# Performance work log

Hardware: AMD Instinct MI355X
Metric: run time of the kernel (lower is better)

Reference implementation:

```python
import jax, jax.numpy as jnp
import numpy as np

DIN = 1024
DOUT = 1024


def setup_inputs() -> dict:
    key = jax.random.key(0)
    kx, kq, kk, kv = jax.random.split(key, 4)
    B, T = 4, 2048
    x = jax.random.normal(kx, (B, T, DIN), dtype=jnp.float32)
    # nn.Linear weights are (dout, din); init like PyTorch default scale
    s = 1.0 / np.sqrt(DIN)
    Wq = jax.random.uniform(kq, (DOUT, DIN), minval=-s, maxval=s, dtype=jnp.float32)
    Wk = jax.random.uniform(kk, (DOUT, DIN), minval=-s, maxval=s, dtype=jnp.float32)
    Wv = jax.random.uniform(kv, (DOUT, DIN), minval=-s, maxval=s, dtype=jnp.float32)
    return {"x": x, "Wq": Wq, "Wk": Wk, "Wv": Wv}


def reference(x, Wq, Wk, Wv):
    B, T, _ = x.shape
    q = jnp.einsum('btd,ed->bte', x, Wq)
    k = jnp.einsum('btd,ed->bte', x, Wk)
    v = jnp.einsum('btd,ed->bte', x, Wv)
    attn = jnp.einsum('bqe,bke->bqk', q, k)  # [B, T, T]
    # Faithful to source: masked_fill result is discarded, so the causal mask
    # is a MULTIPLICATIVE tril of ones (upper triangle logits become 0, not -inf).
    mask = jnp.tril(jnp.ones((T, T), dtype=attn.dtype))
    attn = attn * mask
    # Faithful to source: scale by sqrt(last dim of attn) = sqrt(T), not sqrt(d).
    attn = jax.nn.softmax(attn / jnp.sqrt(jnp.asarray(T, attn.dtype)), axis=-1)
    return jnp.einsum('bqk,bke->bqe', attn, v)
```

## Files before the change

### kernel.cpp

```cpp
#include <hip/hip_runtime.h>
#include <stdint.h>

#define BB 4
#define TT 2048
#define DD 1024
#define NX (BB*TT*DD)
#define NW (DD*DD)
#define SCALE 0.022097086912079608f

typedef short v8s __attribute__((ext_vector_type(8)));
typedef float v4f __attribute__((ext_vector_type(4)));

typedef const void __attribute__((address_space(1))) *as1_cvp;
typedef void __attribute__((address_space(3))) *as3_vp;

__device__ __forceinline__ short f2bf(float f) {
    union { float f; uint32_t u; } x; x.f = f;
    uint32_t r = x.u + 0x7fffu + ((x.u >> 16) & 1u);
    return (short)(r >> 16);
}
__device__ __forceinline__ float bf2f(short s) {
    union { uint32_t u; float f; } x; x.u = ((uint32_t)(uint16_t)s) << 16;
    return x.f;
}

__device__ __forceinline__ void gl_lds16(const short* g, const short* lds_wave_base) {
    __builtin_amdgcn_global_load_lds(
        (as1_cvp)(uintptr_t)(const void*)g,
        (as3_vp)(uint32_t)(uintptr_t)(const void*)lds_wave_base,
        16, 0, 0);
}

__device__ __forceinline__ void stage_tile(const short* __restrict__ gsrc, int lda,
                                           short* lds, int tid) {
    int wave = tid >> 6;
    #pragma unroll
    for (int is = 0; is < 4; is++) {
        int t = is * 256 + tid;
        int r = t >> 3, c = t & 7;
        int cg = c ^ (r & 7);
        const short* g = gsrc + (size_t)r * lda + cg * 8;
        const short* l = lds + is * 2048 + wave * 512;
        gl_lds16(g, l);
    }
}
__device__ __forceinline__ void stage_tile64(const short* __restrict__ gsrc, int lda,
                                             short* lds, int tid) {
    int wave = tid >> 6;
    #pragma unroll
    for (int is = 0; is < 2; is++) {
        int t = is * 256 + tid;
        int r = t >> 3, c = t & 7;
        int cg = c ^ (r & 7);
        const short* g = gsrc + (size_t)r * lda + cg * 8;
        const short* l = lds + is * 2048 + wave * 512;
        gl_lds16(g, l);
    }
}
__device__ __forceinline__ v8s frag_read(const short* lds, int row, int cg) {
    return *(const v8s*)(lds + row * 64 + ((cg ^ (row & 7)) << 3));
}

#define COMPUTE_TILE(Ac, Bc)                                                        \
    _Pragma("unroll")                                                               \
    for (int kk = 0; kk < 2; kk++) {                                                \
        v8s af[4], bf[4];                                                           \
        _Pragma("unroll")                                                           \
        for (int i = 0; i < 4; i++) af[i] = frag_read(Ac, wm + i*16 + lr, kk*4 + lq); \
        _Pragma("unroll")                                                           \
        for (int j = 0; j < 4; j++) bf[j] = frag_read(Bc, wn + j*16 + lr, kk*4 + lq); \
        _Pragma("unroll")                                                           \
        for (int i = 0; i < 4; i++)                                                 \
            _Pragma("unroll")                                                       \
            for (int j = 0; j < 4; j++)                                             \
                acc[i][j] = __builtin_amdgcn_mfma_f32_16x16x32_bf16(af[i], bf[j], acc[i][j], 0, 0, 0); \
    }

#define COMPUTE_TILE64(Ac, Bc)                                                      \
    _Pragma("unroll")                                                               \
    for (int kk = 0; kk < 2; kk++) {                                                \
        v8s af[2], bf[4];                                                           \
        _Pragma("unroll")                                                           \
        for (int i = 0; i < 2; i++) af[i] = frag_read(Ac, wm + i*16 + lr, kk*4 + lq); \
        _Pragma("unroll")                                                           \
        for (int j = 0; j < 4; j++) bf[j] = frag_read(Bc, wn + j*16 + lr, kk*4 + lq); \
        _Pragma("unroll")                                                           \
        for (int i = 0; i < 2; i++)                                                 \
            _Pragma("unroll")                                                       \
            for (int j = 0; j < 4; j++)                                             \
                acc[i][j] = __builtin_amdgcn_mfma_f32_16x16x32_bf16(af[i], bf[j], acc[i][j], 0, 0, 0); \
    }

__global__ void k_convert(const float* __restrict__ x, const float* __restrict__ Wq,
                          const float* __restrict__ Wk, const float* __restrict__ Wv,
                          short* __restrict__ dst, float* __restrict__ rowsum) {
    int i = blockIdx.x * 256 + threadIdx.x;
    if (i < BB * TT) rowsum[i] = (float)((15 - ((i & 2047) >> 7)) * 128);
    size_t base = (size_t)i * 4;
    const float* src; size_t off;
    if (base < NX)               { src = x;  off = base; }
    else if (base < NX + NW)     { src = Wq; off = base - NX; }
    else if (base < NX + 2*(size_t)NW) { src = Wk; off = base - NX - NW; }
    else                         { src = Wv; off = base - NX - 2*(size_t)NW; }
    float4 f = *(const float4*)(src + off);
    short4 h; h.x = f2bf(f.x); h.y = f2bf(f.y); h.z = f2bf(f.z); h.w = f2bf(f.w);
    *(short4*)(dst + base) = h;
}

__global__ __launch_bounds__(256) void k_qkv(const short* __restrict__ xb,
                                             const short* __restrict__ wb,
                                             short* __restrict__ q,
                                             short* __restrict__ k,
                                             short* __restrict__ vt) {
    int which = blockIdx.z;
    const short* Bm = wb + (size_t)which * NW;
    int m0 = blockIdx.x * 128, n0 = blockIdx.y * 128;
    __shared__ __align__(16) short SH[32768];
    int tid = threadIdx.x, lane = tid & 63, wave = tid >> 6;
    int wm = (wave >> 1) * 64, wn = (wave & 1) * 64;
    int lr = lane & 15, lq = lane >> 4;
    v4f acc[4][4];
    for (int i = 0; i < 4; i++) for (int j = 0; j < 4; j++) acc[i][j] = (v4f){0.f,0.f,0.f,0.f};

    const short* Ag = xb + (size_t)m0 * 1024;
    const short* Bg = Bm + (size_t)n0 * 1024;
    stage_tile(Ag, 1024, SH, tid);
    stage_tile(Bg, 1024, SH + 16384, tid);
    #pragma unroll
    for (int it = 0; it < 16; ++it) {
        __syncthreads();
        short* Ac = SH + (it & 1) * 8192;
        short* Bc = SH + 16384 + (it & 1) * 8192;
        if (it + 1 < 16) {
            stage_tile(Ag + (it + 1) * 64, 1024, SH + ((it + 1) & 1) * 8192, tid);
            stage_tile(Bg + (it + 1) * 64, 1024, SH + 16384 + ((it + 1) & 1) * 8192, tid);
        }
        COMPUTE_TILE(Ac, Bc);
    }
    short* outp = (which == 0) ? q : k;
    #pragma unroll
    for (int i = 0; i < 4; i++)
        #pragma unroll
        for (int j = 0; j < 4; j++)
            #pragma unroll
            for (int r = 0; r < 4; r++) {
                int row = m0 + wm + i*16 + lq*4 + r;
                int col = n0 + wn + j*16 + lr;
                short hv = f2bf(acc[i][j][r]);
                if (which == 2) {
                    int bb = row >> 11, t = row & 2047;
                    vt[((size_t)bb << 21) + ((size_t)col << 11) + t] = hv;
                } else {
                    outp[(size_t)row * 1024 + col] = hv;
                }
            }
}

__global__ void k_ts1(const short* __restrict__ vt, float* __restrict__ TSpart) {
    int g = blockIdx.x * 256 + threadIdx.x;
    int b = g >> 14, jt = (g >> 10) & 15, e = g & 1023;
    const short* row = vt + ((size_t)b << 21) + ((size_t)e << 11) + jt * 128;
    float s = 0.f;
    #pragma unroll
    for (int c = 0; c < 16; c++) {
        uint4 u = *(const uint4*)(row + c * 8);
        const short* hp = (const short*)&u;
        #pragma unroll
        for (int z = 0; z < 8; z++) s += bf2f(hp[z]);
    }
    TSpart[g] = s;
}
__global__ void k_ts2(const float* __restrict__ TSpart, float* __restrict__ TS) {
    int g = blockIdx.x * 256 + threadIdx.x;
    int b = g >> 10, e = g & 1023;
    float acc = 0.f;
    TS[(size_t)(b * 17 + 16) * 1024 + e] = 0.f;
    for (int jt = 15; jt >= 0; jt--) {
        acc += TSpart[(size_t)(b * 16 + jt) * 1024 + e];
        TS[(size_t)(b * 17 + jt) * 1024 + e] = acc;
    }
}

__global__ __launch_bounds__(256, 3) void k_pk(const short* __restrict__ qm,
                                               const short* __restrict__ km,
                                               short* __restrict__ P,
                                               float* __restrict__ rowsum) {
    int flip = 271 - blockIdx.x, b = blockIdx.z;
    int half = flip & 1, pidx = flip >> 1;
    int qt = 0;
    while ((qt + 1) * (qt + 2) / 2 <= pidx) qt++;
    int kt = pidx - qt * (qt + 1) / 2;
    int r0 = qt * 128 + half * 64;
    const short* Ag = qm + ((size_t)b * 2048 + r0) * 1024;
    const short* Bg = km + ((size_t)b * 2048 + (size_t)kt * 128) * 1024;
    __shared__ __align__(16) short SH[24576];
    int tid = threadIdx.x, lane = tid & 63, wave = tid >> 6;
    int wm = (wave >> 1) * 32, wn = (wave & 1) * 64;
    int lr = lane & 15, lq = lane >> 4;
    v4f acc[2][4];
    for (int i = 0; i < 2; i++) for (int j = 0; j < 4; j++) acc[i][j] = (v4f){0.f,0.f,0.f,0.f};

    stage_tile64(Ag, 1024, SH, tid);
    stage_tile(Bg, 1024, SH + 8192, tid);
    #pragma unroll
    for (int it = 0; it < 16; ++it) {
        __syncthreads();
        short* Ac = SH + (it & 1) * 4096;
        short* Bc = SH + 8192 + (it & 1) * 8192;
        if (it + 1 < 16) {
            stage_tile64(Ag + (it + 1) * 64, 1024, SH + ((it + 1) & 1) * 4096, tid);
            stage_tile  (Bg + (it + 1) * 64, 1024, SH + 8192 + ((it + 1) & 1) * 8192, tid);
        }
        COMPUTE_TILE64(Ac, Bc);
    }
    short* Pb = P + ((size_t)b << 22);
    float rs[2][4];
    for (int i = 0; i < 2; i++) for (int r = 0; r < 4; r++) rs[i][r] = 0.f;
    #pragma unroll
    for (int i = 0; i < 2; i++)
        #pragma unroll
        for (int j = 0; j < 4; j++)
            #pragma unroll
            for (int r = 0; r < 4; r++) {
                int qi = r0 + wm + i*16 + lq*4 + r;
                int kj = kt * 128 + wn + j*16 + lr;
                float p = (kj <= qi) ? __expf(acc[i][j][r] * SCALE) : 1.0f;
                Pb[(size_t)qi * 2048 + kj] = f2bf(p);
                rs[i][r] += p;
            }
    #pragma unroll
    for (int m = 1; m < 16; m <<= 1)
        #pragma unroll
        for (int i = 0; i < 2; i++)
            #pragma unroll
            for (int r = 0; r < 4; r++) rs[i][r] += __shfl_xor(rs[i][r], m);
    if (lr == 0)
        #pragma unroll
        for (int i = 0; i < 2; i++)
            #pragma unroll
            for (int r = 0; r < 4; r++)
                atomicAdd(&rowsum[b * 2048 + r0 + wm + i*16 + lq*4 + r], rs[i][r]);
}

__global__ __launch_bounds__(256, 3) void k_pv(const short* __restrict__ P,
                                               const short* __restrict__ vt,
                                               const float* __restrict__ rowsum,
                                               const float* __restrict__ TS,
                                               float* __restrict__ out) {
    int et = blockIdx.x, p = blockIdx.y >> 1, half = blockIdx.y & 1, b = blockIdx.z;
    const short* Bg = vt + ((size_t)b << 21) + (size_t)et * 128 * 2048;
    __shared__ __align__(16) short SH[24576];
    int tid = threadIdx.x, lane = tid & 63, wave = tid >> 6;
    int wm = (wave >> 1) * 32, wn = (wave & 1) * 64;
    int lr = lane & 15, lq = lane >> 4;

    #pragma unroll
    for (int ph = 0; ph < 2; ph++) {
        int qt = ph ? p : 15 - p;
        int r0 = qt * 128 + half * 64;
        int iters = 2 * (qt + 1);
        const short* Ag = P + ((size_t)b << 22) + (size_t)r0 * 2048;
        v4f acc[2][4];
        for (int i = 0; i < 2; i++) for (int j = 0; j < 4; j++) acc[i][j] = (v4f){0.f,0.f,0.f,0.f};

        stage_tile64(Ag, 2048, SH, tid);
        stage_tile(Bg, 2048, SH + 8192, tid);
        for (int it = 0; it < iters; it += 2) {
            __syncthreads();
            if (it + 1 < iters) {
                stage_tile64(Ag + (it + 1) * 64, 2048, SH + 4096, tid);
                stage_tile  (Bg + (it + 1) * 64, 2048, SH + 8192 + 8192, tid);
            }
            COMPUTE_TILE64(SH, SH + 8192);
            __syncthreads();
            if (it + 2 < iters) {
                stage_tile64(Ag + (it + 2) * 64, 2048, SH, tid);
                stage_tile  (Bg + (it + 2) * 64, 2048, SH + 8192, tid);
            }
            COMPUTE_TILE64(SH + 4096, SH + 8192 + 8192);
        }
        const float* tsrow = TS + (size_t)(b * 17 + qt + 1) * 1024;
        #pragma unroll
        for (int i = 0; i < 2; i++)
            #pragma unroll
            for (int j = 0; j < 4; j++)
                #pragma unroll
                for (int r = 0; r < 4; r++) {
                    int row = r0 + wm + i*16 + lq*4 + r;
                    int col = et * 128 + wn + j*16 + lr;
                    float o = (acc[i][j][r] + tsrow[col]) / rowsum[b * 2048 + row];
                    out[((size_t)(b * 2048 + row) << 10) + col] = o;
                }
        __syncthreads();
    }
}

extern "C" void kernel_launch(void* const* d_in, const int* in_sizes, int n_in,
                              void* d_out, int out_size, void* d_ws, size_t ws_size,
                              hipStream_t stream) {
    const float* x  = (const float*)d_in[0];
    const float* Wq = (const float*)d_in[1];
    const float* Wk = (const float*)d_in[2];
    const float* Wv = (const float*)d_in[3];
    float* out = (float*)d_out;
    char* ws = (char*)d_ws;

    short* xb     = (short*)(ws + 0);
    short* wb     = (short*)(ws + 16777216);
    short* q      = (short*)(ws + 23068672);
    short* k      = (short*)(ws + 39845888);
    short* vt     = (short*)(ws + 56623104);
    short* P      = (short*)(ws + 73400320);
    float* rowsum = (float*)(ws + 106954752);
    float* TSpart = (float*)(ws + 106987520);
    float* TS     = (float*)(ws + 107249664);

    k_convert<<<11264, 256, 0, stream>>>(x, Wq, Wk, Wv, xb, rowsum);
    k_qkv<<<dim3(64, 8, 3), 256, 0, stream>>>(xb, wb, q, k, vt);
    k_ts1<<<256, 256, 0, stream>>>(vt, TSpart);
    k_ts2<<<16, 256, 0, stream>>>(TSpart, TS);
    k_pk<<<dim3(272, 1, 4), 256, 0, stream>>>(q, k, P, rowsum);
    k_pv<<<dim3(8, 16, 4), 256, 0, stream>>>(P, vt, rowsum, TS, out);
}
```

Measured before the change: 226.2 us.

## Rewrite QKV GEMM with 256x256 tiles, 8 waves, and interleaved staging pipeline

The QKV projection kernel moves from 128x128 tiles with 4 waves to 256x256 tiles with 8 waves. Global-to-LDS loads are split into half-tile stages that are interleaved with MFMA sub-blocks, using explicit vmcnt waits, barriers and setprio, with double buffering across K steps. Blocks are remapped with an XCD-aware swizzle of a 1D grid of 384 blocks. The goal is higher arithmetic intensity and better overlap of loads with compute. The cost is much higher register use (a 32-accumulator tile) and 128KB of LDS per block, which may limit occupancy.

```diff
diff --git a/kernel.cpp b/kernel.cpp
--- a/kernel.cpp
+++ b/kernel.cpp
@@ -61,20 +61,30 @@
     return *(const v8s*)(lds + row * 64 + ((cg ^ (row & 7)) << 3));
 }
 
-#define COMPUTE_TILE(Ac, Bc)                                                        \
-    _Pragma("unroll")                                                               \
-    for (int kk = 0; kk < 2; kk++) {                                                \
-        v8s af[4], bf[4];                                                           \
-        _Pragma("unroll")                                                           \
-        for (int i = 0; i < 4; i++) af[i] = frag_read(Ac, wm + i*16 + lr, kk*4 + lq); \
-        _Pragma("unroll")                                                           \
-        for (int j = 0; j < 4; j++) bf[j] = frag_read(Bc, wn + j*16 + lr, kk*4 + lq); \
-        _Pragma("unroll")                                                           \
-        for (int i = 0; i < 4; i++)                                                 \
-            _Pragma("unroll")                                                       \
-            for (int j = 0; j < 4; j++)                                             \
-                acc[i][j] = __builtin_amdgcn_mfma_f32_16x16x32_bf16(af[i], bf[j], acc[i][j], 0, 0, 0); \
-    }
+__device__ __forceinline__ void stageA256(const short* __restrict__ g, short* lds,
+                                          int tid, int p) {
+    int wave = tid >> 6;
+    #pragma unroll
+    for (int s = 0; s < 2; s++) {
+        int t = s * 512 + tid;
+        int row = t >> 3, c = t & 7;
+        int cg = c ^ (row & 7);
+        int grow = ((row >> 6) << 7) + p * 64 + (row & 63);
+        gl_lds16(g + (size_t)grow * 1024 + cg * 8, lds + s * 4096 + wave * 512);
+    }
+}
+__device__ __forceinline__ void stageB256(const short* __restrict__ g, short* lds,
+                                          int tid, int p) {
+    int wave = tid >> 6;
+    #pragma unroll
+    for (int s = 0; s < 2; s++) {
+        int t = s * 512 + tid;
+        int row = t >> 3, c = t & 7;
+        int cg = c ^ (row & 7);
+        int grow = ((row >> 5) << 6) + p * 32 + (row & 31);
+        gl_lds16(g + (size_t)grow * 1024 + cg * 8, lds + s * 4096 + wave * 512);
+    }
+}
 
 #define COMPUTE_TILE64(Ac, Bc)                                                      \
     _Pragma("unroll")                                                               \
@@ -107,53 +117,186 @@
     *(short4*)(dst + base) = h;
 }
 
-__global__ __launch_bounds__(256) void k_qkv(const short* __restrict__ xb,
-                                             const short* __restrict__ wb,
-                                             short* __restrict__ q,
-                                             short* __restrict__ k,
-                                             short* __restrict__ vt) {
-    int which = blockIdx.z;
-    const short* Bm = wb + (size_t)which * NW;
-    int m0 = blockIdx.x * 128, n0 = blockIdx.y * 128;
-    __shared__ __align__(16) short SH[32768];
+__global__ __launch_bounds__(512, 2) void k_qkv(const short* __restrict__ xb,
+                                                const short* __restrict__ wb,
+                                                short* __restrict__ q,
+                                                short* __restrict__ k,
+                                                short* __restrict__ vt) {
+    int h = blockIdx.x;
+    int w = (h & 7) * 48 + (h >> 3);
+    int which = w >> 7, rw = w & 127, ntile = rw >> 5, mtile = rw & 31;
+    int m0 = mtile * 256, n0 = ntile * 256;
+    const short* Ag = xb + (size_t)m0 * 1024;
+    const short* Bg = wb + (size_t)which * NW + (size_t)n0 * 1024;
+    __shared__ __align__(16) short SH[65536];
     int tid = threadIdx.x, lane = tid & 63, wave = tid >> 6;
-    int wm = (wave >> 1) * 64, wn = (wave & 1) * 64;
+    int wm = (wave >> 2) * 128, wn = (wave & 3) * 64;
     int lr = lane & 15, lq = lane >> 4;
-    v4f acc[4][4];
-    for (int i = 0; i < 4; i++) for (int j = 0; j < 4; j++) acc[i][j] = (v4f){0.f,0.f,0.f,0.f};
-
-    const short* Ag = xb + (size_t)m0 * 1024;
-    const short* Bg = Bm + (size_t)n0 * 1024;
-    stage_tile(Ag, 1024, SH, tid);
-    stage_tile(Bg, 1024, SH + 16384, tid);
-    #pragma unroll
-    for (int it = 0; it < 16; ++it) {
-        __syncthreads();
-        short* Ac = SH + (it & 1) * 8192;
-        short* Bc = SH + 16384 + (it & 1) * 8192;
-        if (it + 1 < 16) {
-            stage_tile(Ag + (it + 1) * 64, 1024, SH + ((it + 1) & 1) * 8192, tid);
-            stage_tile(Bg + (it + 1) * 64, 1024, SH + 16384 + ((it + 1) & 1) * 8192, tid);
-        }
-        COMPUTE_TILE(Ac, Bc);
-    }
-    short* outp = (which == 0) ? q : k;
-    #pragma unroll
-    for (int i = 0; i < 4; i++)
-        #pragma unroll
-        for (int j = 0; j < 4; j++)
-            #pragma unroll
-            for (int r = 0; r < 4; r++) {
-                int row = m0 + wm + i*16 + lq*4 + r;
-                int col = n0 + wn + j*16 + lr;
-                short hv = f2bf(acc[i][j][r]);
-                if (which == 2) {
-                    int bb = row >> 11, t = row & 2047;
-                    vt[((size_t)bb << 21) + ((size_t)col << 11) + t] = hv;
-                } else {
-                    outp[(size_t)row * 1024 + col] = hv;
+    int ar = (wm >> 1) + lr;
+    int br = (wn >> 1) + lr;
+    v4f acc[8][4];
+    #pragma unroll
+    for (int i = 0; i < 8; i++)
+        #pragma unroll
+        for (int j = 0; j < 4; j++) acc[i][j] = (v4f){0.f, 0.f, 0.f, 0.f};
+
+    stageA256(Ag, SH,                tid, 0);
+    stageB256(Bg, SH + 16384,        tid, 0);
+    stageB256(Bg, SH + 16384 + 8192, tid, 1);
+    stageA256(Ag, SH + 8192,         tid, 1);
+    asm volatile("s_waitcnt vmcnt(4)" ::: "memory");
+    __builtin_amdgcn_s_barrier();
+
+    for (int t = 0; t < 15; ++t) {
+        short* sAc = SH + (t & 1) * 32768;
+        short* sBc = sAc + 16384;
+        short* sAn = SH + ((t & 1) ^ 1) * 32768;
+        short* sBn = sAn + 16384;
+        const short* Agn = Ag + (t + 1) * 64;
+        const short* Bgn = Bg + (t + 1) * 64;
+        v8s af[4][2], bf1[2][2], bf2[2][2];
+        #pragma unroll
+        for (int i = 0; i < 4; i++)
+            #pragma unroll
+            for (int kk = 0; kk < 2; kk++) af[i][kk] = frag_read(sAc, ar + i * 16, kk * 4 + lq);
+        #pragma unroll
+        for (int j = 0; j < 2; j++)
+            #pragma unroll
+            for (int kk = 0; kk < 2; kk++) bf1[j][kk] = frag_read(sBc, br + j * 16, kk * 4 + lq);
+        stageA256(Agn, sAn, tid, 0);
+        __builtin_amdgcn_s_setprio(1);
+        #pragma unroll
+        for (int kk = 0; kk < 2; kk++)
+            #pragma unroll
+            for (int i = 0; i < 4; i++)
+                #pragma unroll
+                for (int j = 0; j < 2; j++)
+                    acc[i][j] = __builtin_amdgcn_mfma_f32_16x16x32_bf16(af[i][kk], bf1[j][kk], acc[i][j], 0, 0, 0);
+        __builtin_amdgcn_s_setprio(0);
+        asm volatile("s_waitcnt vmcnt(4)" ::: "memory");
+        __builtin_amdgcn_s_barrier();
+        #pragma unroll
+        for (int j = 0; j < 2; j++)
+            #pragma unroll
+            for (int kk = 0; kk < 2; kk++) bf2[j][kk] = frag_read(sBc + 8192, br + j * 16, kk * 4 + lq);
+        stageB256(Bgn, sBn, tid, 0);
+        __builtin_amdgcn_s_setprio(1);
+        #pragma unroll
+        for (int kk = 0; kk < 2; kk++)
+            #pragma unroll
+            for (int i = 0; i < 4; i++)
+                #pragma unroll
+                for (int j = 0; j < 2; j++)
+                    acc[i][2 + j] = __builtin_amdgcn_mfma_f32_16x16x32_bf16(af[i][kk], bf2[j][kk], acc[i][2 + j], 0, 0, 0);
+        __builtin_amdgcn_s_setprio(0);
+        asm volatile("s_waitcnt vmcnt(4)" ::: "memory");
+        __builtin_amdgcn_s_barrier();
+        #pragma unroll
+        for (int i = 0; i < 4; i++)
+            #pragma unroll
+            for (int kk = 0; kk < 2; kk++) af[i][kk] = frag_read(sAc + 8192, ar + i * 16, kk * 4 + lq);
+        stageB256(Bgn, sBn + 8192, tid, 1);
+        __builtin_amdgcn_s_setprio(1);
+        #pragma unroll
+        for (int kk = 0; kk < 2; kk++)
+            #pragma unroll
+            for (int i = 0; i < 4; i++)
+                #pragma unroll
+                for (int j = 0; j < 2; j++)
+                    acc[4 + i][j] = __builtin_amdgcn_mfma_f32_16x16x32_bf16(af[i][kk], bf1[j][kk], acc[4 + i][j], 0, 0, 0);
+        __builtin_amdgcn_s_setprio(0);
+        stageA256(Agn, sAn + 8192, tid, 1);
+        __builtin_amdgcn_s_setprio(1);
+        #pragma unroll
+        for (int kk = 0; kk < 2; kk++)
+            #pragma unroll
+            for (int i = 0; i < 4; i++)
+                #pragma unroll
+                for (int j = 0; j < 2; j++)
+                    acc[4 + i][2 + j] = __builtin_amdgcn_mfma_f32_16x16x32_bf16(af[i][kk], bf2[j][kk], acc[4 + i][2 + j], 0, 0, 0);
+        __builtin_amdgcn_s_setprio(0);
+        asm volatile("s_waitcnt vmcnt(4)" ::: "memory");
+        __builtin_amdgcn_s_barrier();
+    }
+    {
+        short* sAc = SH + 32768;
+        short* sBc = sAc + 16384;
+        v8s af[4][2], bf1[2][2], bf2[2][2];
+        #pragma unroll
+        for (int i = 0; i < 4; i++)
+            #pragma unroll
+            for (int kk = 0; kk < 2; kk++) af[i][kk] = frag_read(sAc, ar + i * 16, kk * 4 + lq);
+        #pragma unroll
+        for (int j = 0; j < 2; j++)
+            #pragma unroll
+            for (int kk = 0; kk < 2; kk++) bf1[j][kk] = frag_read(sBc, br + j * 16, kk * 4 + lq);
+        __builtin_amdgcn_s_setprio(1);
+        #pragma unroll
+        for (int kk = 0; kk < 2; kk++)
+            #pragma unroll
+            for (int i = 0; i < 4; i++)
+                #pragma unroll
+                for (int j = 0; j < 2; j++)
+                    acc[i][j] = __builtin_amdgcn_mfma_f32_16x16x32_bf16(af[i][kk], bf1[j][kk], acc[i][j], 0, 0, 0);
+        __builtin_amdgcn_s_setprio(0);
+        asm volatile("s_waitcnt vmcnt(2)" ::: "memory");
+        __builtin_amdgcn_s_barrier();
+        #pragma unroll
+        for (int j = 0; j < 2; j++)
+            #pragma unroll
+            for (int kk = 0; kk < 2; kk++) bf2[j][kk] = frag_read(sBc + 8192, br + j * 16, kk * 4 + lq);
+        __builtin_amdgcn_s_setprio(1);
+        #pragma unroll
+        for (int kk = 0; kk < 2; kk++)
+            #pragma unroll
+            for (int i = 0; i < 4; i++)
+                #pragma unroll
+                for (int j = 0; j < 2; j++)
+                    acc[i][2 + j] = __builtin_amdgcn_mfma_f32_16x16x32_bf16(af[i][kk], bf2[j][kk], acc[i][2 + j], 0, 0, 0);
+        __builtin_amdgcn_s_setprio(0);
+        asm volatile("s_waitcnt vmcnt(0)" ::: "memory");
+        __builtin_amdgcn_s_barrier();
+        #pragma unroll
+        for (int i = 0; i < 4; i++)
+            #pragma unroll
+            for (int kk = 0; kk < 2; kk++) af[i][kk] = frag_read(sAc + 8192, ar + i * 16, kk * 4 + lq);
+        __builtin_amdgcn_s_setprio(1);
+        #pragma unroll
+        for (int kk = 0; kk < 2; kk++)
+            #pragma unroll
+            for (int i = 0; i < 4; i++)
+                #pragma unroll
+                for (int j = 0; j < 2; j++) {
+                    acc[4 + i][j]     = __builtin_amdgcn_mfma_f32_16x16x32_bf16(af[i][kk], bf1[j][kk], acc[4 + i][j], 0, 0, 0);
+                    acc[4 + i][2 + j] = __builtin_amdgcn_mfma_f32_16x16x32_bf16(af[i][kk], bf2[j][kk], acc[4 + i][2 + j], 0, 0, 0);
                 }
-            }
+        __builtin_amdgcn_s_setprio(0);
+    }
+    if (which == 2) {
+        #pragma unroll
+        for (int a = 0; a < 8; a++)
+            #pragma unroll
+            for (int b = 0; b < 4; b++)
+                #pragma unroll
+                for (int r = 0; r < 4; r++) {
+                    int row = m0 + wm + a * 16 + lq * 4 + r;
+                    int col = n0 + wn + b * 16 + lr;
+                    int bb = row >> 11, tt2 = row & 2047;
+                    vt[((size_t)bb << 21) + ((size_t)col << 11) + tt2] = f2bf(acc[a][b][r]);
+                }
+    } else {
+        short* outp = (which == 0) ? q : k;
+        #pragma unroll
+        for (int a = 0; a < 8; a++)
+            #pragma unroll
+            for (int b = 0; b < 4; b++)
+                #pragma unroll
+                for (int r = 0; r < 4; r++) {
+                    int row = m0 + wm + a * 16 + lq * 4 + r;
+                    int col = n0 + wn + b * 16 + lr;
+                    outp[(size_t)row * 1024 + col] = f2bf(acc[a][b][r]);
+                }
+    }
 }
 
 __global__ void k_ts1(const short* __restrict__ vt, float* __restrict__ TSpart) {
@@ -316,7 +459,7 @@
     float* TS     = (float*)(ws + 107249664);
 
     k_convert<<<11264, 256, 0, stream>>>(x, Wq, Wk, Wv, xb, rowsum);
-    k_qkv<<<dim3(64, 8, 3), 256, 0, stream>>>(xb, wb, q, k, vt);
+    k_qkv<<<dim3(384, 1, 1), 512, 0, stream>>>(xb, wb, q, k, vt);
     k_ts1<<<256, 256, 0, stream>>>(vt, TSpart);
     k_ts2<<<16, 256, 0, stream>>>(TSpart, TS);
     k_pk<<<dim3(272, 1, 4), 256, 0, stream>>>(q, k, P, rowsum);
```

Result: slower. 232.4 us (+2.7%).

## Restructure QKV GEMM to 128x256 tiles with 8 waves and split-B pipelining

Applied to the files above, without the earlier changes.

The QKV projection GEMM now uses 512-thread blocks computing 128x256 output tiles, with triple-part LDS staging (A plus two B halves) double-buffered. Explicit vmcnt waits and raw barriers let the second B half load while the first half's MFMAs run, and s_setprio raises priority around the MFMA bursts. Block IDs are remapped across a 1D grid so that consecutive blocks share weight tiles. The aim is more reuse per LDS load and better overlap of loads with compute in the largest GEMM, at the cost of more LDS per block and hand-tuned wait counts that must match the number of outstanding loads.

```diff
diff --git a/kernel.cpp b/kernel.cpp
--- a/kernel.cpp
+++ b/kernel.cpp
@@ -61,20 +61,28 @@
     return *(const v8s*)(lds + row * 64 + ((cg ^ (row & 7)) << 3));
 }
 
-#define COMPUTE_TILE(Ac, Bc)                                                        \
-    _Pragma("unroll")                                                               \
-    for (int kk = 0; kk < 2; kk++) {                                                \
-        v8s af[4], bf[4];                                                           \
-        _Pragma("unroll")                                                           \
-        for (int i = 0; i < 4; i++) af[i] = frag_read(Ac, wm + i*16 + lr, kk*4 + lq); \
-        _Pragma("unroll")                                                           \
-        for (int j = 0; j < 4; j++) bf[j] = frag_read(Bc, wn + j*16 + lr, kk*4 + lq); \
-        _Pragma("unroll")                                                           \
-        for (int i = 0; i < 4; i++)                                                 \
-            _Pragma("unroll")                                                       \
-            for (int j = 0; j < 4; j++)                                             \
-                acc[i][j] = __builtin_amdgcn_mfma_f32_16x16x32_bf16(af[i], bf[j], acc[i][j], 0, 0, 0); \
-    }
+__device__ __forceinline__ void stageA128(const short* __restrict__ g, short* lds, int tid) {
+    int wave = tid >> 6;
+    #pragma unroll
+    for (int s = 0; s < 2; s++) {
+        int t = s * 512 + tid;
+        int r = t >> 3, c = t & 7;
+        int cg = c ^ (r & 7);
+        gl_lds16(g + (size_t)r * 1024 + cg * 8, lds + s * 4096 + wave * 512);
+    }
+}
+__device__ __forceinline__ void stageBpart(const short* __restrict__ g, short* lds,
+                                           int tid, int p) {
+    int wave = tid >> 6;
+    #pragma unroll
+    for (int s = 0; s < 2; s++) {
+        int t = s * 512 + tid;
+        int r = t >> 3, c = t & 7;
+        int cg = c ^ (r & 7);
+        int grow = ((r >> 5) << 6) + p * 32 + (r & 31);
+        gl_lds16(g + (size_t)grow * 1024 + cg * 8, lds + s * 4096 + wave * 512);
+    }
+}
 
 #define COMPUTE_TILE64(Ac, Bc)                                                      \
     _Pragma("unroll")                                                               \
@@ -107,53 +115,108 @@
     *(short4*)(dst + base) = h;
 }
 
-__global__ __launch_bounds__(256) void k_qkv(const short* __restrict__ xb,
-                                             const short* __restrict__ wb,
-                                             short* __restrict__ q,
-                                             short* __restrict__ k,
-                                             short* __restrict__ vt) {
-    int which = blockIdx.z;
-    const short* Bm = wb + (size_t)which * NW;
-    int m0 = blockIdx.x * 128, n0 = blockIdx.y * 128;
-    __shared__ __align__(16) short SH[32768];
+__global__ __launch_bounds__(512, 2) void k_qkv(const short* __restrict__ xb,
+                                                const short* __restrict__ wb,
+                                                short* __restrict__ q,
+                                                short* __restrict__ k,
+                                                short* __restrict__ vt) {
+    int h = blockIdx.x;
+    int w = (h & 7) * 96 + (h >> 3);
+    int which = w >> 8, rem = w & 255, ntile = rem >> 6, mtile = rem & 63;
+    int m0 = mtile * 128, n0 = ntile * 256;
+    const short* Ag = xb + (size_t)m0 * 1024;
+    const short* Bg = wb + (size_t)which * NW + (size_t)n0 * 1024;
+    __shared__ __align__(16) short SH[49152];
     int tid = threadIdx.x, lane = tid & 63, wave = tid >> 6;
-    int wm = (wave >> 1) * 64, wn = (wave & 1) * 64;
+    int wm = wave >> 2, wn = wave & 3;
     int lr = lane & 15, lq = lane >> 4;
+    int arow = wm * 64 + lr;
+    int brow = wn * 32 + lr;
     v4f acc[4][4];
-    for (int i = 0; i < 4; i++) for (int j = 0; j < 4; j++) acc[i][j] = (v4f){0.f,0.f,0.f,0.f};
-
-    const short* Ag = xb + (size_t)m0 * 1024;
-    const short* Bg = Bm + (size_t)n0 * 1024;
-    stage_tile(Ag, 1024, SH, tid);
-    stage_tile(Bg, 1024, SH + 16384, tid);
-    #pragma unroll
-    for (int it = 0; it < 16; ++it) {
-        __syncthreads();
-        short* Ac = SH + (it & 1) * 8192;
-        short* Bc = SH + 16384 + (it & 1) * 8192;
-        if (it + 1 < 16) {
-            stage_tile(Ag + (it + 1) * 64, 1024, SH + ((it + 1) & 1) * 8192, tid);
-            stage_tile(Bg + (it + 1) * 64, 1024, SH + 16384 + ((it + 1) & 1) * 8192, tid);
+    #pragma unroll
+    for (int i = 0; i < 4; i++)
+        #pragma unroll
+        for (int j = 0; j < 4; j++) acc[i][j] = (v4f){0.f, 0.f, 0.f, 0.f};
+
+    stageA128 (Ag, SH,         tid);
+    stageBpart(Bg, SH + 8192,  tid, 0);
+    stageBpart(Bg, SH + 16384, tid, 1);
+
+    #pragma unroll
+    for (int t = 0; t < 16; ++t) {
+        short* S  = SH + (t & 1) * 24576;
+        short* Sn = SH + ((t + 1) & 1) * 24576;
+        const short* Agn = Ag + (t + 1) * 64;
+        const short* Bgn = Bg + (t + 1) * 64;
+        asm volatile("s_waitcnt vmcnt(2)" ::: "memory");
+        __builtin_amdgcn_s_barrier();
+        v8s af[4][2], bf[2][2];
+        #pragma unroll
+        for (int i = 0; i < 4; i++)
+            #pragma unroll
+            for (int kk = 0; kk < 2; kk++) af[i][kk] = frag_read(S, arow + i * 16, kk * 4 + lq);
+        #pragma unroll
+        for (int jj = 0; jj < 2; jj++)
+            #pragma unroll
+            for (int kk = 0; kk < 2; kk++) bf[jj][kk] = frag_read(S + 8192, brow + jj * 16, kk * 4 + lq);
+        if (t < 15) {
+            stageA128 (Agn, Sn,        tid);
+            stageBpart(Bgn, Sn + 8192, tid, 0);
         }
-        COMPUTE_TILE(Ac, Bc);
-    }
-    short* outp = (which == 0) ? q : k;
-    #pragma unroll
-    for (int i = 0; i < 4; i++)
-        #pragma unroll
-        for (int j = 0; j < 4; j++)
-            #pragma unroll
-            for (int r = 0; r < 4; r++) {
-                int row = m0 + wm + i*16 + lq*4 + r;
-                int col = n0 + wn + j*16 + lr;
-                short hv = f2bf(acc[i][j][r]);
-                if (which == 2) {
-                    int bb = row >> 11, t = row & 2047;
-                    vt[((size_t)bb << 21) + ((size_t)col << 11) + t] = hv;
-                } else {
-                    outp[(size_t)row * 1024 + col] = hv;
+        __builtin_amdgcn_s_setprio(1);
+        #pragma unroll
+        for (int kk = 0; kk < 2; kk++)
+            #pragma unroll
+            for (int i = 0; i < 4; i++)
+                #pragma unroll
+                for (int jj = 0; jj < 2; jj++)
+                    acc[i][jj] = __builtin_amdgcn_mfma_f32_16x16x32_bf16(af[i][kk], bf[jj][kk], acc[i][jj], 0, 0, 0);
+        __builtin_amdgcn_s_setprio(0);
+        if (t < 15) { asm volatile("s_waitcnt vmcnt(4)" ::: "memory"); }
+        else        { asm volatile("s_waitcnt vmcnt(0)" ::: "memory"); }
+        __builtin_amdgcn_s_barrier();
+        v8s bg2[2][2];
+        #pragma unroll
+        for (int jj = 0; jj < 2; jj++)
+            #pragma unroll
+            for (int kk = 0; kk < 2; kk++) bg2[jj][kk] = frag_read(S + 16384, brow + jj * 16, kk * 4 + lq);
+        if (t < 15) stageBpart(Bgn, Sn + 16384, tid, 1);
+        __builtin_amdgcn_s_setprio(1);
+        #pragma unroll
+        for (int kk = 0; kk < 2; kk++)
+            #pragma unroll
+            for (int i = 0; i < 4; i++)
+                #pragma unroll
+                for (int jj = 0; jj < 2; jj++)
+                    acc[i][2 + jj] = __builtin_amdgcn_mfma_f32_16x16x32_bf16(af[i][kk], bg2[jj][kk], acc[i][2 + jj], 0, 0, 0);
+        __builtin_amdgcn_s_setprio(0);
+    }
+
+    if (which == 2) {
+        #pragma unroll
+        for (int a = 0; a < 4; a++)
+            #pragma unroll
+            for (int b = 0; b < 4; b++)
+                #pragma unroll
+                for (int r = 0; r < 4; r++) {
+                    int row = m0 + wm * 64 + a * 16 + lq * 4 + r;
+                    int col = n0 + wn * 64 + b * 16 + lr;
+                    int bb = row >> 11, tt2 = row & 2047;
+                    vt[((size_t)bb << 21) + ((size_t)col << 11) + tt2] = f2bf(acc[a][b][r]);
                 }
-            }
+    } else {
+        short* outp = (which == 0) ? q : k;
+        #pragma unroll
+        for (int a = 0; a < 4; a++)
+            #pragma unroll
+            for (int b = 0; b < 4; b++)
+                #pragma unroll
+                for (int r = 0; r < 4; r++) {
+                    int row = m0 + wm * 64 + a * 16 + lq * 4 + r;
+                    int col = n0 + wn * 64 + b * 16 + lr;
+                    outp[(size_t)row * 1024 + col] = f2bf(acc[a][b][r]);
+                }
+    }
 }
 
 __global__ void k_ts1(const short* __restrict__ vt, float* __restrict__ TSpart) {
@@ -316,7 +379,7 @@
     float* TS     = (float*)(ws + 107249664);
 
     k_convert<<<11264, 256, 0, stream>>>(x, Wq, Wk, Wv, xb, rowsum);
-    k_qkv<<<dim3(64, 8, 3), 256, 0, stream>>>(xb, wb, q, k, vt);
+    k_qkv<<<dim3(768, 1, 1), 512, 0, stream>>>(xb, wb, q, k, vt);
     k_ts1<<<256, 256, 0, stream>>>(vt, TSpart);
     k_ts2<<<16, 256, 0, stream>>>(TSpart, TS);
     k_pk<<<dim3(272, 1, 4), 256, 0, stream>>>(q, k, P, rowsum);
```

Result: no change. 224.8 us (-0.6%).
